# Kernel tuning notes

Measured on AMD Instinct MI355X. Metric: run time of the kernel, lower is better.

## Reference

```python
import jax, jax.numpy as jnp
import numpy as np

B, S, H = 4, 1024, 2048
E = 16            # num_experts
K = 2             # num_experts_per_token
I = 1024          # per-expert intermediate_dim
N_SHARED = 2
I_SHARED = I * N_SHARED
RATIO = 0.1       # shared_expert_ratio
EPS = 1e-9


def _swiglu(x, wg, wu, wd):
    # SwiGLU, bias=False: down( silu(gate(x)) * up(x) )
    return (jax.nn.silu(x @ wg) * (x @ wu)) @ wd


def setup_inputs() -> dict:
    key = jax.random.key(0)
    ks = jax.random.split(key, 9)
    scale = 0.02
    x = jax.random.normal(ks[0], (B, S, H), dtype=jnp.float32)
    centroids = jax.random.normal(ks[1], (E, H), dtype=jnp.float32)  # nn.Parameter(randn)
    gate_bias = jnp.zeros((E,), dtype=jnp.float32)
    # shared expert SwiGLU weights (intermediate = I * n_shared_experts)
    wg_s = jax.random.normal(ks[2], (H, I_SHARED), dtype=jnp.float32) * scale
    wu_s = jax.random.normal(ks[3], (H, I_SHARED), dtype=jnp.float32) * scale
    wd_s = jax.random.normal(ks[4], (I_SHARED, H), dtype=jnp.float32) * scale
    # routed experts, stacked [E, ...]
    wg = jax.random.normal(ks[5], (E, H, I), dtype=jnp.float32) * scale
    wu = jax.random.normal(ks[6], (E, H, I), dtype=jnp.float32) * scale
    wd = jax.random.normal(ks[7], (E, I, H), dtype=jnp.float32) * scale
    return {"x": x, "centroids": centroids, "gate_bias": gate_bias,
            "wg_s": wg_s, "wu_s": wu_s, "wd_s": wd_s,
            "wg": wg, "wu": wu, "wd": wd}


def reference(x, centroids, gate_bias, wg_s, wu_s, wd_s, wg, wu, wd):
    # 1) shared expert on ALL tokens, scaled by ratio
    shared = _swiglu(x, wg_s, wu_s, wd_s) * RATIO          # [B,S,H]
    # 2) centroid affinity (DeepSeek-V3 sigmoid gating)
    affinity = jax.nn.sigmoid(jnp.einsum('bsh,eh->bse', x, centroids))  # [B,S,E]
    # 3) bias used ONLY for selection
    biased = affinity + gate_bias
    _, top_idx = jax.lax.top_k(biased, K)                  # [B,S,K]
    # 4) clean weights from unbiased affinity, normalized to sum 1
    top_aff = jnp.take_along_axis(affinity, top_idx, axis=-1)  # [B,S,K]
    weights = top_aff / (top_aff.sum(-1, keepdims=True) + EPS)
    # 5) combine-mask: per-token per-expert weight (0 if not selected)
    mask = (jax.nn.one_hot(top_idx, E, dtype=x.dtype) * weights[..., None]).sum(-2)  # [B,S,E]
    # 6) expert compute + weighted combine; loop over fixed small E avoids
    #    materializing a [B,S,E,H] tensor
    routed = jnp.zeros_like(x)
    for e in range(E):
        routed = routed + mask[..., e:e + 1] * _swiglu(x, wg[e], wu[e], wd[e])
    return shared + routed
```

## Files before the change

kernel.cpp:

```cpp
#include <hip/hip_runtime.h>
#include <hip/hip_bf16.h>

typedef unsigned short u16;
typedef unsigned int u32;
typedef unsigned long long u64;
typedef __attribute__((ext_vector_type(8))) short short8;
typedef __attribute__((ext_vector_type(4))) float f32x4;

#define TOKENS 4096
#define HDIM 2048
#define NEXP 16
#define IDIM 1024
#define ISH 2048
#define MAXTILES 80
#define NCHUNK 128

#define AS1(p) ((const __attribute__((address_space(1))) u32*)(p))
#define AS3(p) ((__attribute__((address_space(3))) u32*)(p))

__device__ __forceinline__ u16 f2b(float f) {
    u32 u = __float_as_uint(f);
    u32 r = u + 0x7fffu + ((u >> 16) & 1u);
    return (u16)(r >> 16);
}

__global__ __launch_bounds__(256) void convert_x_kernel(const float* __restrict__ x,
                                                        u16* __restrict__ xb) {
    size_t i = ((size_t)blockIdx.x * 256 + threadIdx.x) * 8;
    float4 a = *(const float4*)(x + i);
    float4 b = *(const float4*)(x + i + 4);
    u32 p0 = (u32)f2b(a.x) | ((u32)f2b(a.y) << 16);
    u32 p1 = (u32)f2b(a.z) | ((u32)f2b(a.w) << 16);
    u32 p2 = (u32)f2b(b.x) | ((u32)f2b(b.y) << 16);
    u32 p3 = (u32)f2b(b.z) | ((u32)f2b(b.w) << 16);
    uint4 o = make_uint4(p0, p1, p2, p3);
    *(uint4*)(xb + i) = o;
}

__global__ __launch_bounds__(256) void route_kernel(const float* __restrict__ x,
                                                    const float* __restrict__ cent,
                                                    const float* __restrict__ bias,
                                                    int* __restrict__ top_e,
                                                    float* __restrict__ top_w) {
    __shared__ alignas(16) float cs[8 * 2048];
    int lane = threadIdx.x & 63;
    int wv = threadIdx.x >> 6;
    int t = blockIdx.x * 4 + wv;
    const float4* xp4 = (const float4*)(x + (size_t)t * HDIM);
    float4 xr[8];
#pragma unroll
    for (int i = 0; i < 8; i++) xr[i] = xp4[lane + 64 * i];
    float aff[16];
#pragma unroll
    for (int ph = 0; ph < 2; ph++) {
        if (ph) __syncthreads();
        const float* sbase = cent + (size_t)(ph * 8 + wv * 2) * HDIM;
        float* dbase = cs + (size_t)wv * 2 * HDIM;
#pragma unroll
        for (int i = 0; i < 16; i++) {
            __builtin_amdgcn_global_load_lds(AS1(sbase + i * 256 + lane * 4),
                                             AS3(dbase + i * 256), 16, 0, 0);
        }
        __syncthreads();
#pragma unroll
        for (int e = 0; e < 8; e++) {
            const float4* cp = (const float4*)cs + (size_t)e * 512;
            float s = 0.f;
#pragma unroll
            for (int i = 0; i < 8; i++) {
                float4 cv = cp[lane + 64 * i];
                s += xr[i].x * cv.x;
                s += xr[i].y * cv.y;
                s += xr[i].z * cv.z;
                s += xr[i].w * cv.w;
            }
#pragma unroll
            for (int off = 32; off > 0; off >>= 1) s += __shfl_xor(s, off, 64);
            aff[ph * 8 + e] = 1.f / (1.f + expf(-s));
        }
    }
    float b0 = -1e30f, b1 = -1e30f, a0 = 0.f, a1 = 0.f;
    int e0 = -1, e1 = -1;
#pragma unroll
    for (int e = 0; e < 16; e++) {
        float v = aff[e] + bias[e];
        if (v > b0) {
            b1 = b0; e1 = e0; a1 = a0;
            b0 = v; e0 = e; a0 = aff[e];
        } else if (v > b1) {
            b1 = v; e1 = e; a1 = aff[e];
        }
    }
    float inv = 1.f / (a0 + a1 + 1e-9f);
    if (lane == 0) {
        top_e[2 * t] = e0; top_w[2 * t] = a0 * inv;
        top_e[2 * t + 1] = e1; top_w[2 * t + 1] = a1 * inv;
    }
}

__global__ __launch_bounds__(1024) void build_kernel(
    const int* __restrict__ top_e, const float* __restrict__ top_w,
    int* __restrict__ counts, int* __restrict__ offsets, int* __restrict__ ntiles,
    int* __restrict__ tile_e, int* __restrict__ tile_m,
    int* __restrict__ list_tok, float* __restrict__ list_w) {
    __shared__ int cnt[NCHUNK][16];
    __shared__ int offs_s[16];
    __shared__ int totals[16];
    int tid = threadIdx.x;
    int lane = tid & 63, wv = tid >> 6;
    for (int c = wv; c < NCHUNK; c += 16) {
        int v = top_e[c * 64 + lane];
#pragma unroll
        for (int e = 0; e < 16; e++) {
            u64 m = __ballot(v == e);
            if (lane == 0) cnt[c][e] = (int)__popcll(m);
        }
    }
    __syncthreads();
    if (tid < 16) {
        int s = 0;
        for (int c = 0; c < NCHUNK; c++) s += cnt[c][tid];
        totals[tid] = s;
        counts[tid] = s;
    }
    __syncthreads();
    if (tid == 0) {
        int r = 0, nt = 0;
        for (int e = 0; e < 16; e++) {
            offs_s[e] = r;
            offsets[e] = r;
            int ce = totals[e];
            int tcnt = (ce + 127) >> 7;
            for (int m = 0; m < tcnt; m++) {
                tile_e[nt] = e;
                tile_m[nt] = m;
                nt++;
            }
            r += ce;
        }
        *ntiles = nt;
    }
    __syncthreads();
    if (tid < 16) {
        int r = offs_s[tid];
        for (int c = 0; c < NCHUNK; c++) {
            int v = cnt[c][tid];
            cnt[c][tid] = r;
            r += v;
        }
    }
    __syncthreads();
    for (int c = wv; c < NCHUNK; c += 16) {
        int i = c * 64 + lane;
        int v = top_e[i];
        int rank = 0;
#pragma unroll
        for (int e = 0; e < 16; e++) {
            u64 m = __ballot(v == e);
            if (v == e) rank = (int)__popcll(m & ((1ull << lane) - 1ull));
        }
        int slot = cnt[c][v] + rank;
        list_tok[slot] = i >> 1;
        list_w[slot] = top_w[i];
    }
}

__global__ __launch_bounds__(256) void conv_w_kernel(const float* __restrict__ W,
                                                     u16* __restrict__ Wt, int K, int N) {
    int nt = blockIdx.x, kc = blockIdx.y;
    size_t mato = (size_t)blockIdx.z * K * N;
    const float* Wm = W + mato;
    u16* Wtm = Wt + mato;
    int ksB = K >> 5;
    __shared__ u16 Ls[64 * 40];
    int t = threadIdx.x;
    int kr = t >> 3, ng = t & 7;
    int nn = t >> 2, seg = t & 3;
    int g = seg ^ ((nn >> 2) & 3);
#pragma unroll
    for (int s = 0; s < 8; s++) {
        int kb = kc * 256 + s * 32;
        const float* src = Wm + (size_t)(kb + kr) * N + nt * 64 + ng * 8;
        float4 f0 = *(const float4*)src;
        float4 f1 = *(const float4*)(src + 4);
        __syncthreads();
        const float* p0 = (const float*)&f0;
        const float* p1 = (const float*)&f1;
#pragma unroll
        for (int l = 0; l < 4; l++) Ls[(8 * ng + l) * 40 + kr] = f2b(p0[l]);
#pragma unroll
        for (int l = 0; l < 4; l++) Ls[(8 * ng + 4 + l) * 40 + kr] = f2b(p1[l]);
        __syncthreads();
        const u16* lp = &Ls[nn * 40 + g * 8];
        u32 w0 = (u32)lp[0] | ((u32)lp[1] << 16);
        u32 w1 = (u32)lp[2] | ((u32)lp[3] << 16);
        u32 w2 = (u32)lp[4] | ((u32)lp[5] << 16);
        u32 w3 = (u32)lp[6] | ((u32)lp[7] << 16);
        uint4 o = make_uint4(w0, w1, w2, w3);
        *(uint4*)(Wtm + (size_t)(nt * ksB + (kb >> 5)) * 2048 + t * 8) = o;
    }
}

__global__ __launch_bounds__(256) void gemm_gateup(
    const u16* __restrict__ A, const u16* __restrict__ BgAll, const u16* __restrict__ BuAll,
    u16* __restrict__ hout, int Kd, int Nout, const int* __restrict__ counts,
    const int* __restrict__ offsets, const int* __restrict__ ntiles,
    const int* __restrict__ tile_e, const int* __restrict__ tile_m,
    const int* __restrict__ list_tok, int routed) {
    int cnt = TOKENS, base = 0, m0;
    const u16* Bg = BgAll;
    const u16* Bu = BuAll;
    if (routed) {
        int ti = blockIdx.x;
        if (ti >= *ntiles) return;
        int e = tile_e[ti];
        m0 = tile_m[ti] * 128;
        cnt = counts[e];
        base = offsets[e];
        size_t off = (size_t)e * Kd * Nout;
        Bg += off; Bu += off;
    } else {
        m0 = blockIdx.x * 128;
    }
    int ksB = Kd >> 5;
    __shared__ alignas(16) u16 As[128 * 32];
    __shared__ alignas(16) u16 Bgs[64 * 32];
    __shared__ alignas(16) u16 Bus[64 * 32];
    int tid = threadIdx.x;
    int lane = tid & 63, wv = tid >> 6;
    int quad = lane >> 4, mr = lane & 15;
    int n0 = blockIdx.y * 64;
    int gk = (tid & 3) ^ ((tid >> 4) & 3);
    int mg0 = min(m0 + (tid >> 2), cnt - 1);
    int mg1 = min(m0 + 64 + (tid >> 2), cnt - 1);
    size_t sr0 = routed ? (size_t)list_tok[base + mg0] : (size_t)mg0;
    size_t sr1 = routed ? (size_t)list_tok[base + mg1] : (size_t)mg1;
    const u16* ap0 = A + sr0 * Kd + gk * 8;
    const u16* ap1 = A + sr1 * Kd + gk * 8;
    const u16* bgp = Bg + (size_t)blockIdx.y * ksB * 2048 + tid * 8;
    const u16* bup = Bu + (size_t)blockIdx.y * ksB * 2048 + tid * 8;
    u16* AsW = As + wv * 512;
    u16* AsW2 = As + 2048 + wv * 512;
    u16* BgsW = Bgs + wv * 512;
    u16* BusW = Bus + wv * 512;
    int xq = quad ^ ((mr >> 2) & 3);
    const short8* a0p = (const short8*)(As + ((32 * wv + mr) * 4 + xq) * 8);
    const short8* a1p = (const short8*)(As + ((32 * wv + 16 + mr) * 4 + xq) * 8);
    f32x4 accg[2][4], accu[2][4];
#pragma unroll
    for (int i = 0; i < 2; i++)
#pragma unroll
        for (int j = 0; j < 4; j++) { accg[i][j] = (f32x4)0.f; accu[i][j] = (f32x4)0.f; }

    for (int ks = 0; ks < ksB; ks++) {
        __syncthreads();
        __builtin_amdgcn_global_load_lds(AS1(ap0), AS3(AsW), 16, 0, 0);
        __builtin_amdgcn_global_load_lds(AS1(ap1), AS3(AsW2), 16, 0, 0);
        __builtin_amdgcn_global_load_lds(AS1(bgp), AS3(BgsW), 16, 0, 0);
        __builtin_amdgcn_global_load_lds(AS1(bup), AS3(BusW), 16, 0, 0);
        ap0 += 32; ap1 += 32; bgp += 2048; bup += 2048;
        __syncthreads();
        short8 a0 = *a0p;
        short8 a1 = *a1p;
#pragma unroll
        for (int j = 0; j < 4; j++) {
            short8 bg = *(const short8*)(Bgs + (64 * j + mr * 4 + xq) * 8);
            short8 bu = *(const short8*)(Bus + (64 * j + mr * 4 + xq) * 8);
            accg[0][j] = __builtin_amdgcn_mfma_f32_16x16x32_bf16(a0, bg, accg[0][j], 0, 0, 0);
            accg[1][j] = __builtin_amdgcn_mfma_f32_16x16x32_bf16(a1, bg, accg[1][j], 0, 0, 0);
            accu[0][j] = __builtin_amdgcn_mfma_f32_16x16x32_bf16(a0, bu, accu[0][j], 0, 0, 0);
            accu[1][j] = __builtin_amdgcn_mfma_f32_16x16x32_bf16(a1, bu, accu[1][j], 0, 0, 0);
        }
    }
#pragma unroll
    for (int i = 0; i < 2; i++)
#pragma unroll
        for (int j = 0; j < 4; j++)
#pragma unroll
            for (int r = 0; r < 4; r++) {
                int m = m0 + 32 * wv + 16 * i + quad * 4 + r;
                if (m < cnt) {
                    float gv = accg[i][j][r], uv = accu[i][j][r];
                    float h = gv / (1.f + expf(-gv)) * uv;
                    int n = n0 + 16 * j + mr;
                    hout[(size_t)(base + m) * Nout + n] = f2b(h);
                }
            }
}

__global__ __launch_bounds__(256) void gemm_down(
    const u16* __restrict__ A, const u16* __restrict__ BAll, float* __restrict__ out,
    int Kd, const int* __restrict__ counts, const int* __restrict__ offsets,
    const int* __restrict__ ntiles, const int* __restrict__ tile_e,
    const int* __restrict__ tile_m, const int* __restrict__ list_tok,
    const float* __restrict__ list_w, int routed) {
    int cnt = TOKENS, base = 0, m0;
    const u16* B = BAll;
    if (routed) {
        int ti = blockIdx.x;
        if (ti >= *ntiles) return;
        int e = tile_e[ti];
        m0 = tile_m[ti] * 128;
        cnt = counts[e];
        base = offsets[e];
        B += (size_t)e * Kd * HDIM;
    } else {
        m0 = blockIdx.x * 128;
    }
    int ksB = Kd >> 5;
    __shared__ alignas(16) u16 As[128 * 32];
    __shared__ alignas(16) u16 Bs[64 * 32];
    int tid = threadIdx.x;
    int lane = tid & 63, wv = tid >> 6;
    int quad = lane >> 4, mr = lane & 15;
    int n0 = blockIdx.y * 64;
    int gk = (tid & 3) ^ ((tid >> 4) & 3);
    int mg0 = base + min(m0 + (tid >> 2), cnt - 1);
    int mg1 = base + min(m0 + 64 + (tid >> 2), cnt - 1);
    const u16* ap0 = A + (size_t)mg0 * Kd + gk * 8;
    const u16* ap1 = A + (size_t)mg1 * Kd + gk * 8;
    const u16* bp = B + (size_t)blockIdx.y * ksB * 2048 + tid * 8;
    u16* AsW = As + wv * 512;
    u16* AsW2 = As + 2048 + wv * 512;
    u16* BsW = Bs + wv * 512;
    int xq = quad ^ ((mr >> 2) & 3);
    const short8* a0p = (const short8*)(As + ((32 * wv + mr) * 4 + xq) * 8);
    const short8* a1p = (const short8*)(As + ((32 * wv + 16 + mr) * 4 + xq) * 8);
    f32x4 acc[2][4];
#pragma unroll
    for (int i = 0; i < 2; i++)
#pragma unroll
        for (int j = 0; j < 4; j++) acc[i][j] = (f32x4)0.f;

    for (int ks = 0; ks < ksB; ks++) {
        __syncthreads();
        __builtin_amdgcn_global_load_lds(AS1(ap0), AS3(AsW), 16, 0, 0);
        __builtin_amdgcn_global_load_lds(AS1(ap1), AS3(AsW2), 16, 0, 0);
        __builtin_amdgcn_global_load_lds(AS1(bp), AS3(BsW), 16, 0, 0);
        ap0 += 32; ap1 += 32; bp += 2048;
        __syncthreads();
        short8 a0 = *a0p;
        short8 a1 = *a1p;
#pragma unroll
        for (int j = 0; j < 4; j++) {
            short8 b = *(const short8*)(Bs + (64 * j + mr * 4 + xq) * 8);
            acc[0][j] = __builtin_amdgcn_mfma_f32_16x16x32_bf16(a0, b, acc[0][j], 0, 0, 0);
            acc[1][j] = __builtin_amdgcn_mfma_f32_16x16x32_bf16(a1, b, acc[1][j], 0, 0, 0);
        }
    }
#pragma unroll
    for (int i = 0; i < 2; i++)
#pragma unroll
        for (int j = 0; j < 4; j++)
#pragma unroll
            for (int r = 0; r < 4; r++) {
                int m = m0 + 32 * wv + 16 * i + quad * 4 + r;
                if (m >= cnt) continue;
                int n = n0 + 16 * j + mr;
                float v = acc[i][j][r];
                if (routed) {
                    int tok = list_tok[base + m];
                    atomicAdd(out + (size_t)tok * HDIM + n, list_w[base + m] * v);
                } else {
                    out[(size_t)m * HDIM + n] = 0.1f * v;
                }
            }
}

extern "C" void kernel_launch(void* const* d_in, const int* in_sizes, int n_in,
                              void* d_out, int out_size, void* d_ws, size_t ws_size,
                              hipStream_t stream) {
    const float* x = (const float*)d_in[0];
    const float* cent = (const float*)d_in[1];
    const float* bias = (const float*)d_in[2];
    const float* wgs = (const float*)d_in[3];
    const float* wus = (const float*)d_in[4];
    const float* wds = (const float*)d_in[5];
    const float* wg = (const float*)d_in[6];
    const float* wu = (const float*)d_in[7];
    const float* wd = (const float*)d_in[8];
    float* out = (float*)d_out;
    char* ws = (char*)d_ws;

    size_t off_wtgs = 0;
    size_t off_wtus = off_wtgs + (size_t)HDIM * ISH * 2;
    size_t off_wtds = off_wtus + (size_t)HDIM * ISH * 2;
    size_t off_wtg = off_wtds + (size_t)ISH * HDIM * 2;
    size_t off_wtu = off_wtg + (size_t)NEXP * HDIM * IDIM * 2;
    size_t off_wtd = off_wtu + (size_t)NEXP * HDIM * IDIM * 2;
    size_t off_xbf = off_wtd + (size_t)NEXP * IDIM * HDIM * 2;
    size_t off_hsh = off_xbf + (size_t)TOKENS * HDIM * 2;
    size_t off_hrt = off_hsh + (size_t)TOKENS * ISH * 2;
    size_t off_meta = off_hrt + (size_t)2 * TOKENS * IDIM * 2;
    size_t need = off_meta + (1 << 20);
    if (ws_size < need) return;

    u16* Wt_gs = (u16*)(ws + off_wtgs);
    u16* Wt_us = (u16*)(ws + off_wtus);
    u16* Wt_ds = (u16*)(ws + off_wtds);
    u16* Wt_g = (u16*)(ws + off_wtg);
    u16* Wt_u = (u16*)(ws + off_wtu);
    u16* Wt_d = (u16*)(ws + off_wtd);
    u16* x_bf = (u16*)(ws + off_xbf);
    u16* h_sh = (u16*)(ws + off_hsh);
    u16* h_rt = (u16*)(ws + off_hrt);
    int* counts = (int*)(ws + off_meta);
    int* offsets = counts + 16;
    int* ntiles = offsets + 16;
    int* tile_e = ntiles + 16;
    int* tile_m = tile_e + MAXTILES;
    int* top_e = tile_m + MAXTILES;
    int* top_s = top_e + 2 * TOKENS;
    float* top_w = (float*)(top_s + 2 * TOKENS);
    int* list_tok = (int*)(top_w + 2 * TOKENS);
    float* list_w = (float*)(list_tok + 2 * TOKENS);

    convert_x_kernel<<<TOKENS * HDIM / (256 * 8), 256, 0, stream>>>(x, x_bf);
    route_kernel<<<TOKENS / 4, 256, 0, stream>>>(x, cent, bias, top_e, top_w);
    build_kernel<<<1, 1024, 0, stream>>>(top_e, top_w, counts, offsets, ntiles, tile_e,
                                         tile_m, list_tok, list_w);

    conv_w_kernel<<<dim3(ISH / 64, HDIM / 256, 1), 256, 0, stream>>>(wgs, Wt_gs, HDIM, ISH);
    conv_w_kernel<<<dim3(ISH / 64, HDIM / 256, 1), 256, 0, stream>>>(wus, Wt_us, HDIM, ISH);
    conv_w_kernel<<<dim3(HDIM / 64, ISH / 256, 1), 256, 0, stream>>>(wds, Wt_ds, ISH, HDIM);
    conv_w_kernel<<<dim3(IDIM / 64, HDIM / 256, NEXP), 256, 0, stream>>>(wg, Wt_g, HDIM, IDIM);
    conv_w_kernel<<<dim3(IDIM / 64, HDIM / 256, NEXP), 256, 0, stream>>>(wu, Wt_u, HDIM, IDIM);
    conv_w_kernel<<<dim3(HDIM / 64, IDIM / 256, NEXP), 256, 0, stream>>>(wd, Wt_d, IDIM, HDIM);

    gemm_gateup<<<dim3(TOKENS / 128, ISH / 64, 1), 256, 0, stream>>>(
        x_bf, Wt_gs, Wt_us, h_sh, HDIM, ISH, nullptr, nullptr, nullptr, nullptr, nullptr,
        nullptr, 0);
    gemm_down<<<dim3(TOKENS / 128, HDIM / 64, 1), 256, 0, stream>>>(
        h_sh, Wt_ds, out, ISH, nullptr, nullptr, nullptr, nullptr, nullptr, nullptr, nullptr, 0);
    gemm_gateup<<<dim3(MAXTILES, IDIM / 64, 1), 256, 0, stream>>>(
        x_bf, Wt_g, Wt_u, h_rt, HDIM, IDIM, counts, offsets, ntiles, tile_e, tile_m,
        list_tok, 1);
    gemm_down<<<dim3(MAXTILES, HDIM / 64, 1), 256, 0, stream>>>(
        h_rt, Wt_d, out, IDIM, counts, offsets, ntiles, tile_e, tile_m, list_tok, list_w, 1);
}
```

Measured before the change: 988.0 us.

## Triple-buffer LDS tiles in gate/up and down GEMMs with async prefetch

```diff
diff --git a/kernel.cpp b/kernel.cpp
--- a/kernel.cpp
+++ b/kernel.cpp
@@ -222,10 +222,10 @@
     } else {
         m0 = blockIdx.x * 128;
     }
-    int ksB = Kd >> 5;
-    __shared__ alignas(16) u16 As[128 * 32];
-    __shared__ alignas(16) u16 Bgs[64 * 32];
-    __shared__ alignas(16) u16 Bus[64 * 32];
+    int nk = Kd >> 5;
+    __shared__ alignas(16) u16 As[3][128 * 32];
+    __shared__ alignas(16) u16 Bgs[3][64 * 32];
+    __shared__ alignas(16) u16 Bus[3][64 * 32];
     int tid = threadIdx.x;
     int lane = tid & 63, wv = tid >> 6;
     int quad = lane >> 4, mr = lane & 15;
@@ -237,41 +237,58 @@
     size_t sr1 = routed ? (size_t)list_tok[base + mg1] : (size_t)mg1;
     const u16* ap0 = A + sr0 * Kd + gk * 8;
     const u16* ap1 = A + sr1 * Kd + gk * 8;
-    const u16* bgp = Bg + (size_t)blockIdx.y * ksB * 2048 + tid * 8;
-    const u16* bup = Bu + (size_t)blockIdx.y * ksB * 2048 + tid * 8;
-    u16* AsW = As + wv * 512;
-    u16* AsW2 = As + 2048 + wv * 512;
-    u16* BgsW = Bgs + wv * 512;
-    u16* BusW = Bus + wv * 512;
+    const u16* bgp = Bg + (size_t)blockIdx.y * nk * 2048 + tid * 8;
+    const u16* bup = Bu + (size_t)blockIdx.y * nk * 2048 + tid * 8;
     int xq = quad ^ ((mr >> 2) & 3);
-    const short8* a0p = (const short8*)(As + ((32 * wv + mr) * 4 + xq) * 8);
-    const short8* a1p = (const short8*)(As + ((32 * wv + 16 + mr) * 4 + xq) * 8);
     f32x4 accg[2][4], accu[2][4];
 #pragma unroll
     for (int i = 0; i < 2; i++)
 #pragma unroll
         for (int j = 0; j < 4; j++) { accg[i][j] = (f32x4)0.f; accu[i][j] = (f32x4)0.f; }
 
-    for (int ks = 0; ks < ksB; ks++) {
-        __syncthreads();
-        __builtin_amdgcn_global_load_lds(AS1(ap0), AS3(AsW), 16, 0, 0);
-        __builtin_amdgcn_global_load_lds(AS1(ap1), AS3(AsW2), 16, 0, 0);
-        __builtin_amdgcn_global_load_lds(AS1(bgp), AS3(BgsW), 16, 0, 0);
-        __builtin_amdgcn_global_load_lds(AS1(bup), AS3(BusW), 16, 0, 0);
-        ap0 += 32; ap1 += 32; bgp += 2048; bup += 2048;
-        __syncthreads();
-        short8 a0 = *a0p;
-        short8 a1 = *a1p;
+#define STAGE_GU(b)                                                                     \
+    do {                                                                                \
+        __builtin_amdgcn_global_load_lds(AS1(ap0), AS3(&As[b][wv * 512]), 16, 0, 0);    \
+        __builtin_amdgcn_global_load_lds(AS1(ap1), AS3(&As[b][2048 + wv * 512]), 16, 0, \
+                                         0);                                            \
+        __builtin_amdgcn_global_load_lds(AS1(bgp), AS3(&Bgs[b][wv * 512]), 16, 0, 0);   \
+        __builtin_amdgcn_global_load_lds(AS1(bup), AS3(&Bus[b][wv * 512]), 16, 0, 0);   \
+        ap0 += 32; ap1 += 32; bgp += 2048; bup += 2048;                                 \
+    } while (0)
+
+    STAGE_GU(0);
+    STAGE_GU(1);
+    asm volatile("s_waitcnt vmcnt(4)" ::: "memory");
+    __builtin_amdgcn_s_barrier();
+
+    int cur = 0;
+    for (int ks = 0; ks < nk; ks++) {
+        int nxt = cur + 2;
+        if (nxt >= 3) nxt -= 3;
+        if (ks + 2 < nk) STAGE_GU(nxt);
+        const u16* Asc = As[cur];
+        const u16* Bgc = Bgs[cur];
+        const u16* Buc = Bus[cur];
+        short8 a0 = *(const short8*)(Asc + ((32 * wv + mr) * 4 + xq) * 8);
+        short8 a1 = *(const short8*)(Asc + ((32 * wv + 16 + mr) * 4 + xq) * 8);
 #pragma unroll
         for (int j = 0; j < 4; j++) {
-            short8 bg = *(const short8*)(Bgs + (64 * j + mr * 4 + xq) * 8);
-            short8 bu = *(const short8*)(Bus + (64 * j + mr * 4 + xq) * 8);
+            short8 bg = *(const short8*)(Bgc + (64 * j + mr * 4 + xq) * 8);
+            short8 bu = *(const short8*)(Buc + (64 * j + mr * 4 + xq) * 8);
             accg[0][j] = __builtin_amdgcn_mfma_f32_16x16x32_bf16(a0, bg, accg[0][j], 0, 0, 0);
             accg[1][j] = __builtin_amdgcn_mfma_f32_16x16x32_bf16(a1, bg, accg[1][j], 0, 0, 0);
             accu[0][j] = __builtin_amdgcn_mfma_f32_16x16x32_bf16(a0, bu, accu[0][j], 0, 0, 0);
             accu[1][j] = __builtin_amdgcn_mfma_f32_16x16x32_bf16(a1, bu, accu[1][j], 0, 0, 0);
         }
-    }
+        if (ks + 2 < nk)
+            asm volatile("s_waitcnt vmcnt(4)" ::: "memory");
+        else
+            asm volatile("s_waitcnt vmcnt(0)" ::: "memory");
+        __builtin_amdgcn_s_barrier();
+        cur = cur + 1 == 3 ? 0 : cur + 1;
+    }
+#undef STAGE_GU
+
 #pragma unroll
     for (int i = 0; i < 2; i++)
 #pragma unroll
@@ -307,9 +324,9 @@
     } else {
         m0 = blockIdx.x * 128;
     }
-    int ksB = Kd >> 5;
-    __shared__ alignas(16) u16 As[128 * 32];
-    __shared__ alignas(16) u16 Bs[64 * 32];
+    int nk = Kd >> 5;
+    __shared__ alignas(16) u16 As[3][128 * 32];
+    __shared__ alignas(16) u16 Bs[3][64 * 32];
     int tid = threadIdx.x;
     int lane = tid & 63, wv = tid >> 6;
     int quad = lane >> 4, mr = lane & 15;
@@ -319,35 +336,52 @@
     int mg1 = base + min(m0 + 64 + (tid >> 2), cnt - 1);
     const u16* ap0 = A + (size_t)mg0 * Kd + gk * 8;
     const u16* ap1 = A + (size_t)mg1 * Kd + gk * 8;
-    const u16* bp = B + (size_t)blockIdx.y * ksB * 2048 + tid * 8;
-    u16* AsW = As + wv * 512;
-    u16* AsW2 = As + 2048 + wv * 512;
-    u16* BsW = Bs + wv * 512;
+    const u16* bp = B + (size_t)blockIdx.y * nk * 2048 + tid * 8;
     int xq = quad ^ ((mr >> 2) & 3);
-    const short8* a0p = (const short8*)(As + ((32 * wv + mr) * 4 + xq) * 8);
-    const short8* a1p = (const short8*)(As + ((32 * wv + 16 + mr) * 4 + xq) * 8);
     f32x4 acc[2][4];
 #pragma unroll
     for (int i = 0; i < 2; i++)
 #pragma unroll
         for (int j = 0; j < 4; j++) acc[i][j] = (f32x4)0.f;
 
-    for (int ks = 0; ks < ksB; ks++) {
-        __syncthreads();
-        __builtin_amdgcn_global_load_lds(AS1(ap0), AS3(AsW), 16, 0, 0);
-        __builtin_amdgcn_global_load_lds(AS1(ap1), AS3(AsW2), 16, 0, 0);
-        __builtin_amdgcn_global_load_lds(AS1(bp), AS3(BsW), 16, 0, 0);
-        ap0 += 32; ap1 += 32; bp += 2048;
-        __syncthreads();
-        short8 a0 = *a0p;
-        short8 a1 = *a1p;
+#define STAGE_D(b)                                                                      \
+    do {                                                                                \
+        __builtin_amdgcn_global_load_lds(AS1(ap0), AS3(&As[b][wv * 512]), 16, 0, 0);    \
+        __builtin_amdgcn_global_load_lds(AS1(ap1), AS3(&As[b][2048 + wv * 512]), 16, 0, \
+                                         0);                                            \
+        __builtin_amdgcn_global_load_lds(AS1(bp), AS3(&Bs[b][wv * 512]), 16, 0, 0);     \
+        ap0 += 32; ap1 += 32; bp += 2048;                                               \
+    } while (0)
+
+    STAGE_D(0);
+    STAGE_D(1);
+    asm volatile("s_waitcnt vmcnt(3)" ::: "memory");
+    __builtin_amdgcn_s_barrier();
+
+    int cur = 0;
+    for (int ks = 0; ks < nk; ks++) {
+        int nxt = cur + 2;
+        if (nxt >= 3) nxt -= 3;
+        if (ks + 2 < nk) STAGE_D(nxt);
+        const u16* Asc = As[cur];
+        const u16* Bc = Bs[cur];
+        short8 a0 = *(const short8*)(Asc + ((32 * wv + mr) * 4 + xq) * 8);
+        short8 a1 = *(const short8*)(Asc + ((32 * wv + 16 + mr) * 4 + xq) * 8);
 #pragma unroll
         for (int j = 0; j < 4; j++) {
-            short8 b = *(const short8*)(Bs + (64 * j + mr * 4 + xq) * 8);
+            short8 b = *(const short8*)(Bc + (64 * j + mr * 4 + xq) * 8);
             acc[0][j] = __builtin_amdgcn_mfma_f32_16x16x32_bf16(a0, b, acc[0][j], 0, 0, 0);
             acc[1][j] = __builtin_amdgcn_mfma_f32_16x16x32_bf16(a1, b, acc[1][j], 0, 0, 0);
         }
-    }
+        if (ks + 2 < nk)
+            asm volatile("s_waitcnt vmcnt(3)" ::: "memory");
+        else
+            asm volatile("s_waitcnt vmcnt(0)" ::: "memory");
+        __builtin_amdgcn_s_barrier();
+        cur = cur + 1 == 3 ? 0 : cur + 1;
+    }
+#undef STAGE_D
+
 #pragma unroll
     for (int i = 0; i < 2; i++)
 #pragma unroll
```

Result: no change. 1.005 ms (+1.7%).
